# Optimization experiments

Hardware: AMD Instinct MI355X
Metric: run time of the kernel (lower is better)

The kernel has to match this reference:

```python
import jax, jax.numpy as jnp
import numpy as np

N_TOKEN = 267735
D_EMBED = 1024
D_PROJ = 1024
DIV_VAL = 4
CUTOFF_ENDS = [0, 20000, 40000, 200000, N_TOKEN]
EMB_SCALE = D_PROJ ** 0.5
INIT_STD = 0.02


def setup_inputs() -> dict:
    key = jax.random.key(0)
    ks = jax.random.split(key, 9)
    inp = jax.random.randint(ks[0], (4, 4096), 0, N_TOKEN, dtype=jnp.int32)
    out = {"inp": inp}
    for i in range(4):
        l, r = CUTOFF_ENDS[i], CUTOFF_ENDS[i + 1]
        d_i = D_EMBED // DIV_VAL ** i  # 1024, 256, 64, 16
        tbl = jax.random.normal(ks[1 + i], (r - l, d_i), dtype=jnp.float32)
        # padding_idx=1: row 1 is zero-initialized in torch nn.Embedding
        tbl = tbl.at[1].set(0.0)
        out[f"emb{i}"] = tbl
        out[f"proj{i}"] = jax.random.normal(ks[5 + i], (D_PROJ, d_i), dtype=jnp.float32) * INIT_STD
    return out


def reference(inp, emb0, emb1, emb2, emb3, proj0, proj1, proj2, proj3):
    tables = [emb0, emb1, emb2, emb3]
    projs = [proj0, proj1, proj2, proj3]
    flat = inp.reshape(-1)                                  # [N]
    out = jnp.zeros((flat.shape[0], D_PROJ), dtype=emb0.dtype)
    for i in range(4):
        l, r = CUTOFF_ENDS[i], CUTOFF_ENDS[i + 1]
        mask = (flat >= l) & (flat < r)                     # [N] bool
        local = jnp.clip(flat - l, 0, r - l - 1)            # in-range local idx
        e_i = tables[i][local]                              # [N, d_i] gather
        p_i = jnp.einsum('nd,pd->np', e_i, projs[i])        # [N, D_PROJ]
        out = out + jnp.where(mask[:, None], p_i, 0.0)      # scatter-by-mask
    out = out * EMB_SCALE
    return out.reshape(*inp.shape, D_PROJ)
```

## Files before the change

kernel.cpp:

```cpp
#include <hip/hip_runtime.h>
#include <hip/hip_bf16.h>

#define DPROJ 1024

typedef float  f32x4  __attribute__((ext_vector_type(4)));
typedef short  bf16x8 __attribute__((ext_vector_type(8)));

__device__ __forceinline__ unsigned pk2(float a, float b) {
    __hip_bfloat162 h = __float22bfloat162_rn(make_float2(a, b));
    unsigned r; __builtin_memcpy(&r, &h, 4); return r;
}

__global__ __launch_bounds__(1024) void k_classify(
    const int* __restrict__ inp, int n,
    int* __restrict__ cnt, int* __restrict__ lists)
{
    __shared__ uint2 s[1024];
    const int tid = threadIdx.x;
    const int pt  = (n + 1023) >> 10;
    const int t0  = tid * pt;

    int v[16];
    unsigned cp = 0;
    uint2 mine = make_uint2(0u, 0u);
    for (int j = 0; j < pt; ++j) {
        int t = t0 + j, c = 0;
        if (t < n) {
            int x = inp[t]; v[j] = x;
            c = (x >= 20000) + (x >= 40000) + (x >= 200000);
            if      (c == 0) mine.x += 1u;
            else if (c == 1) mine.x += 1u << 16;
            else if (c == 2) mine.y += 1u;
            else             mine.y += 1u << 16;
        } else v[j] = 0;
        cp |= (unsigned)c << (2 * j);
    }
    s[tid] = mine;
    for (int off = 1; off < 1024; off <<= 1) {
        __syncthreads();
        uint2 add = make_uint2(0u, 0u);
        if (tid >= off) add = s[tid - off];
        __syncthreads();
        s[tid].x += add.x; s[tid].y += add.y;
    }
    __syncthreads();
    uint2 tot = s[1023];
    uint2 inc = s[tid];
    unsigned run[4] = { (inc.x & 0xffffu) - (mine.x & 0xffffu),
                        (inc.x >> 16)     - (mine.x >> 16),
                        (inc.y & 0xffffu) - (mine.y & 0xffffu),
                        (inc.y >> 16)     - (mine.y >> 16) };
    if (tid == 0) {
        cnt[0] = (int)(tot.x & 0xffffu); cnt[1] = (int)(tot.x >> 16);
        cnt[2] = (int)(tot.y & 0xffffu); cnt[3] = (int)(tot.y >> 16);
    }
    const int cut[4] = {0, 20000, 40000, 200000};
    for (int j = 0; j < pt; ++j) {
        int t = t0 + j;
        if (t >= n) break;
        int c = (int)((cp >> (2 * j)) & 3u);
        int l = v[j] - cut[c];
        unsigned pos = run[c]++;
        lists[c * n + (int)pos] = (int)(((unsigned)t << 18) | (unsigned)l);
    }
}

__global__ __launch_bounds__(256, 4) void k_gemm(
    const int* __restrict__ cnt, const int* __restrict__ lists, int n,
    const float* __restrict__ e0, const float* __restrict__ p0,
    const float* __restrict__ e1, const float* __restrict__ p1,
    const float* __restrict__ e2, const float* __restrict__ p2,
    const float* __restrict__ e3, const float* __restrict__ p3,
    float* __restrict__ out)
{
    constexpr int TM = 64, TN = 128, KC = 32, STR = 40;

    const int z     = blockIdx.z;
    const int count = cnt[z];
    const int row0  = blockIdx.y * TM;
    if (row0 >= count) return;

    const float* emb  = (z == 0) ? e0 : (z == 1) ? e1 : (z == 2) ? e2 : e3;
    const float* proj = (z == 0) ? p0 : (z == 1) ? p1 : (z == 2) ? p2 : p3;
    const int    K    = (z == 0) ? 1024 : (z == 1) ? 256 : (z == 2) ? 64 : 16;
    const int*   list = lists + (size_t)z * n;
    const int    col0 = blockIdx.x * TN;

    __shared__ int   s_tok[TM];
    __shared__ int   s_loc[TM];
    __shared__ short e_s[TM * STR];
    __shared__ short p_s[TN * STR];

    const int tid = threadIdx.x;
    if (tid < TM) {
        int r = row0 + tid;
        if (r < count) {
            unsigned pk = (unsigned)list[r];
            s_tok[tid] = (int)(pk >> 18);
            s_loc[tid] = (int)(pk & 0x3FFFFu);
        } else { s_tok[tid] = -1; s_loc[tid] = -1; }
    }
    __syncthreads();

    const int  erow = tid >> 2, egrp = tid & 3;
    const int  eloc = s_loc[erow];
    const bool ev   = (eloc >= 0);
    const size_t ebase = ev ? (size_t)eloc * K : 0;

    const int wave = tid >> 6, lane = tid & 63;
    const int lm = lane & 15, quad = lane >> 4;

    f32x4 acc[8];
    #pragma unroll
    for (int i = 0; i < 8; ++i) acc[i] = (f32x4){0.f, 0.f, 0.f, 0.f};

    for (int kb = 0; kb < K; kb += KC) {
        if (kb) __syncthreads();

        {
            float f[8] = {0.f, 0.f, 0.f, 0.f, 0.f, 0.f, 0.f, 0.f};
            int ko = kb + egrp * 8;
            if (ev && ko < K) {
                float4 a = *(const float4*)&emb[ebase + ko];
                float4 b = *(const float4*)&emb[ebase + ko + 4];
                f[0] = a.x; f[1] = a.y; f[2] = a.z; f[3] = a.w;
                f[4] = b.x; f[5] = b.y; f[6] = b.z; f[7] = b.w;
            }
            uint4 q; q.x = pk2(f[0], f[1]); q.y = pk2(f[2], f[3]);
                     q.z = pk2(f[4], f[5]); q.w = pk2(f[6], f[7]);
            *(uint4*)&e_s[erow * STR + egrp * 8] = q;
        }
        #pragma unroll
        for (int it = 0; it < 2; ++it) {
            int u    = tid + it * 256;
            int prow = u >> 2, pgrp = u & 3;
            int ko   = kb + pgrp * 8;
            float f[8] = {0.f, 0.f, 0.f, 0.f, 0.f, 0.f, 0.f, 0.f};
            if (ko < K) {
                const float* src = &proj[(size_t)(col0 + prow) * K + ko];
                float4 a = *(const float4*)src;
                float4 b = *(const float4*)(src + 4);
                f[0] = a.x; f[1] = a.y; f[2] = a.z; f[3] = a.w;
                f[4] = b.x; f[5] = b.y; f[6] = b.z; f[7] = b.w;
            }
            uint4 q; q.x = pk2(f[0], f[1]); q.y = pk2(f[2], f[3]);
                     q.z = pk2(f[4], f[5]); q.w = pk2(f[6], f[7]);
            *(uint4*)&p_s[prow * STR + pgrp * 8] = q;
        }
        __syncthreads();

        bf16x8 af = *(const bf16x8*)&e_s[(wave * 16 + lm) * STR + quad * 8];
        #pragma unroll
        for (int ns = 0; ns < 8; ++ns) {
            bf16x8 bf = *(const bf16x8*)&p_s[(ns * 16 + lm) * STR + quad * 8];
            acc[ns] = __builtin_amdgcn_mfma_f32_16x16x32_bf16(af, bf, acc[ns], 0, 0, 0);
        }
    }

    int toks[4];
    #pragma unroll
    for (int r = 0; r < 4; ++r) toks[r] = s_tok[wave * 16 + quad * 4 + r];
    #pragma unroll
    for (int ns = 0; ns < 8; ++ns) {
        int col = col0 + ns * 16 + lm;
        #pragma unroll
        for (int r = 0; r < 4; ++r) {
            if (toks[r] >= 0)
                out[(size_t)toks[r] * DPROJ + col] = acc[ns][r] * 32.f;
        }
    }
}

extern "C" void kernel_launch(void* const* d_in, const int* in_sizes, int n_in,
                              void* d_out, int out_size, void* d_ws, size_t ws_size,
                              hipStream_t stream) {
    const int*   inp = (const int*)d_in[0];
    const float* e0  = (const float*)d_in[1];
    const float* p0  = (const float*)d_in[2];
    const float* e1  = (const float*)d_in[3];
    const float* p1  = (const float*)d_in[4];
    const float* e2  = (const float*)d_in[5];
    const float* p2  = (const float*)d_in[6];
    const float* e3  = (const float*)d_in[7];
    const float* p3  = (const float*)d_in[8];
    float* out = (float*)d_out;
    const int n = in_sizes[0];

    int* cnt   = (int*)d_ws;
    int* lists = cnt + 4;

    k_classify<<<1, 1024, 0, stream>>>(inp, n, cnt, lists);

    dim3 grid(DPROJ / 128, (n + 63) / 64, 4);
    k_gemm<<<grid, 256, 0, stream>>>(cnt, lists, n, e0, p0, e1, p1, e2, p2, e3, p3, out);
}
```

Before: 262.6 us.

## Parallelize token bucketing, pre-convert projections to bf16, double-buffer GEMM loads

```diff
diff --git a/kernel.cpp b/kernel.cpp
--- a/kernel.cpp
+++ b/kernel.cpp
@@ -11,85 +11,86 @@
     unsigned r; __builtin_memcpy(&r, &h, 4); return r;
 }
 
-__global__ __launch_bounds__(1024) void k_classify(
+__device__ __forceinline__ void gll16(const void* g, void* l) {
+    __builtin_amdgcn_global_load_lds(
+        (const __attribute__((address_space(1))) void*)g,
+        (__attribute__((address_space(3))) void*)l, 16, 0, 0);
+}
+
+__global__ __launch_bounds__(256) void k_prep(
     const int* __restrict__ inp, int n,
-    int* __restrict__ cnt, int* __restrict__ lists)
+    int* __restrict__ cnt, int* __restrict__ lists,
+    const float* __restrict__ p0, const float* __restrict__ p1,
+    const float* __restrict__ p2, const float* __restrict__ p3,
+    short* __restrict__ pb0, short* __restrict__ pb1,
+    short* __restrict__ pb2, short* __restrict__ pb3)
 {
-    __shared__ uint2 s[1024];
     const int tid = threadIdx.x;
-    const int pt  = (n + 1023) >> 10;
-    const int t0  = tid * pt;
-
-    int v[16];
-    unsigned cp = 0;
-    uint2 mine = make_uint2(0u, 0u);
-    for (int j = 0; j < pt; ++j) {
-        int t = t0 + j, c = 0;
+    const int b   = blockIdx.x;
+    const int CB  = (n + 255) >> 8;
+    if (b < CB) {
+        const int t = b * 256 + tid;
+        int c = -1, l = 0;
         if (t < n) {
-            int x = inp[t]; v[j] = x;
+            const int x = inp[t];
             c = (x >= 20000) + (x >= 40000) + (x >= 200000);
-            if      (c == 0) mine.x += 1u;
-            else if (c == 1) mine.x += 1u << 16;
-            else if (c == 2) mine.y += 1u;
-            else             mine.y += 1u << 16;
-        } else v[j] = 0;
-        cp |= (unsigned)c << (2 * j);
-    }
-    s[tid] = mine;
-    for (int off = 1; off < 1024; off <<= 1) {
-        __syncthreads();
-        uint2 add = make_uint2(0u, 0u);
-        if (tid >= off) add = s[tid - off];
-        __syncthreads();
-        s[tid].x += add.x; s[tid].y += add.y;
-    }
-    __syncthreads();
-    uint2 tot = s[1023];
-    uint2 inc = s[tid];
-    unsigned run[4] = { (inc.x & 0xffffu) - (mine.x & 0xffffu),
-                        (inc.x >> 16)     - (mine.x >> 16),
-                        (inc.y & 0xffffu) - (mine.y & 0xffffu),
-                        (inc.y >> 16)     - (mine.y >> 16) };
-    if (tid == 0) {
-        cnt[0] = (int)(tot.x & 0xffffu); cnt[1] = (int)(tot.x >> 16);
-        cnt[2] = (int)(tot.y & 0xffffu); cnt[3] = (int)(tot.y >> 16);
-    }
-    const int cut[4] = {0, 20000, 40000, 200000};
-    for (int j = 0; j < pt; ++j) {
-        int t = t0 + j;
-        if (t >= n) break;
-        int c = (int)((cp >> (2 * j)) & 3u);
-        int l = v[j] - cut[c];
-        unsigned pos = run[c]++;
-        lists[c * n + (int)pos] = (int)(((unsigned)t << 18) | (unsigned)l);
+            l = x - ((c == 0) ? 0 : (c == 1) ? 20000 : (c == 2) ? 40000 : 200000);
+        }
+        const int lane = tid & 63;
+        int pos = 0;
+        #pragma unroll
+        for (int cc = 0; cc < 4; ++cc) {
+            const unsigned long long mk = __ballot(c == cc);
+            if (c == cc) {
+                const int lead = __ffsll(mk) - 1;
+                int base = 0;
+                if (lane == lead) base = atomicAdd(&cnt[cc], (int)__popcll(mk));
+                base = __shfl(base, lead);
+                pos  = base + (int)__popcll(mk & ((1ull << lane) - 1ull));
+            }
+        }
+        if (t < n) lists[c * n + pos] = (int)(((unsigned)t << 18) | (unsigned)l);
+    } else {
+        const long g = (long)(b - CB) * 256 + tid;
+        const float* src; short* dst; long lo;
+        if      (g < 131072) { src = p0; dst = pb0; lo = g; }
+        else if (g < 163840) { src = p1; dst = pb1; lo = g - 131072; }
+        else if (g < 172032) { src = p2; dst = pb2; lo = g - 163840; }
+        else if (g < 174080) { src = p3; dst = pb3; lo = g - 172032; }
+        else return;
+        const float4 a = *(const float4*)(src + lo * 8);
+        const float4 c4 = *(const float4*)(src + lo * 8 + 4);
+        uint4 q; q.x = pk2(a.x, a.y);   q.y = pk2(a.z, a.w);
+                 q.z = pk2(c4.x, c4.y); q.w = pk2(c4.z, c4.w);
+        *(uint4*)(dst + lo * 8) = q;
     }
 }
 
 __global__ __launch_bounds__(256, 4) void k_gemm(
     const int* __restrict__ cnt, const int* __restrict__ lists, int n,
-    const float* __restrict__ e0, const float* __restrict__ p0,
-    const float* __restrict__ e1, const float* __restrict__ p1,
-    const float* __restrict__ e2, const float* __restrict__ p2,
-    const float* __restrict__ e3, const float* __restrict__ p3,
+    const float* __restrict__ e0, const float* __restrict__ e1,
+    const float* __restrict__ e2, const float* __restrict__ e3,
+    const short* __restrict__ pb0, const short* __restrict__ pb1,
+    const short* __restrict__ pb2, const short* __restrict__ pb3,
     float* __restrict__ out)
 {
-    constexpr int TM = 64, TN = 128, KC = 32, STR = 40;
+    constexpr int TM = 64, TN = 128, KC = 32, ESTR = 40;
 
     const int z     = blockIdx.z;
     const int count = cnt[z];
     const int row0  = blockIdx.y * TM;
     if (row0 >= count) return;
 
-    const float* emb  = (z == 0) ? e0 : (z == 1) ? e1 : (z == 2) ? e2 : e3;
-    const float* proj = (z == 0) ? p0 : (z == 1) ? p1 : (z == 2) ? p2 : p3;
-    const int    K    = (z == 0) ? 1024 : (z == 1) ? 256 : (z == 2) ? 64 : 16;
-    const int*   list = lists + (size_t)z * n;
-    const int    col0 = blockIdx.x * TN;
+    const float* emb = (z == 0) ? e0  : (z == 1) ? e1  : (z == 2) ? e2  : e3;
+    const short* pb  = (z == 0) ? pb0 : (z == 1) ? pb1 : (z == 2) ? pb2 : pb3;
+    const int    K   = (z == 0) ? 1024 : (z == 1) ? 256 : (z == 2) ? 64 : 16;
+    const int*  list = lists + (size_t)z * n;
+    const int   col0 = blockIdx.x * TN;
 
     __shared__ int   s_tok[TM];
     __shared__ int   s_loc[TM];
-    __shared__ short e_s[TM * STR];
-    __shared__ short p_s[TN * STR];
+    __shared__ short e_s[2][TM * ESTR];
+    __shared__ short p_s[2][4 * TN * 8];
 
     const int tid = threadIdx.x;
     if (tid < TM) {
@@ -102,71 +103,93 @@
     }
     __syncthreads();
 
-    const int  erow = tid >> 2, egrp = tid & 3;
-    const int  eloc = s_loc[erow];
-    const bool ev   = (eloc >= 0);
-    const size_t ebase = ev ? (size_t)eloc * K : 0;
-
     const int wave = tid >> 6, lane = tid & 63;
     const int lm = lane & 15, quad = lane >> 4;
+
+    const int erow = tid >> 2, egrp = tid & 3;
+    const int eloc = s_loc[erow];
+    const bool ev  = (eloc >= 0);
+    const float* ebase = emb + (ev ? (size_t)eloc * K : 0) + egrp * 8;
+    const int eoff = erow * ESTR + egrp * 8;
+    short* ebuf = (short*)e_s;
+    short* pbuf = (short*)p_s;
+
+    const short* pg0 = pb + (size_t)(col0 +      lane) * K + wave * 8;
+    const short* pg1 = pb + (size_t)(col0 + 64 + lane) * K + wave * 8;
+    const int pdoff0 = wave * 128 * 8;
+    const int pdoff1 = wave * 128 * 8 + 64 * 8;
 
     f32x4 acc[8];
     #pragma unroll
     for (int i = 0; i < 8; ++i) acc[i] = (f32x4){0.f, 0.f, 0.f, 0.f};
 
-    for (int kb = 0; kb < K; kb += KC) {
-        if (kb) __syncthreads();
-
-        {
-            float f[8] = {0.f, 0.f, 0.f, 0.f, 0.f, 0.f, 0.f, 0.f};
-            int ko = kb + egrp * 8;
-            if (ev && ko < K) {
-                float4 a = *(const float4*)&emb[ebase + ko];
-                float4 b = *(const float4*)&emb[ebase + ko + 4];
-                f[0] = a.x; f[1] = a.y; f[2] = a.z; f[3] = a.w;
-                f[4] = b.x; f[5] = b.y; f[6] = b.z; f[7] = b.w;
+    const int nt = (K + KC - 1) / KC;
+    float ef[8];
+
+    {
+        const bool v = ev && (egrp * 8 < K);
+        if (v) {
+            float4 a = *(const float4*)(ebase);
+            float4 b = *(const float4*)(ebase + 4);
+            ef[0] = a.x; ef[1] = a.y; ef[2] = a.z; ef[3] = a.w;
+            ef[4] = b.x; ef[5] = b.y; ef[6] = b.z; ef[7] = b.w;
+        } else {
+            #pragma unroll
+            for (int j = 0; j < 8; ++j) ef[j] = 0.f;
+        }
+        gll16(pg0, pbuf + pdoff0);
+        gll16(pg1, pbuf + pdoff1);
+        uint4 q; q.x = pk2(ef[0], ef[1]); q.y = pk2(ef[2], ef[3]);
+                 q.z = pk2(ef[4], ef[5]); q.w = pk2(ef[6], ef[7]);
+        *(uint4*)(ebuf + eoff) = q;
+    }
+    __syncthreads();
+
+    for (int t = 0; t < nt; ++t) {
+        const int  cur = t & 1;
+        const int  kn  = (t + 1) * KC;
+        const bool pf  = (kn < K);
+        if (pf) {
+            const bool v = ev && (kn + egrp * 8 < K);
+            if (v) {
+                const float* s = ebase + kn;
+                float4 a = *(const float4*)(s);
+                float4 b = *(const float4*)(s + 4);
+                ef[0] = a.x; ef[1] = a.y; ef[2] = a.z; ef[3] = a.w;
+                ef[4] = b.x; ef[5] = b.y; ef[6] = b.z; ef[7] = b.w;
+            } else {
+                #pragma unroll
+                for (int j = 0; j < 8; ++j) ef[j] = 0.f;
             }
-            uint4 q; q.x = pk2(f[0], f[1]); q.y = pk2(f[2], f[3]);
-                     q.z = pk2(f[4], f[5]); q.w = pk2(f[6], f[7]);
-            *(uint4*)&e_s[erow * STR + egrp * 8] = q;
-        }
-        #pragma unroll
-        for (int it = 0; it < 2; ++it) {
-            int u    = tid + it * 256;
-            int prow = u >> 2, pgrp = u & 3;
-            int ko   = kb + pgrp * 8;
-            float f[8] = {0.f, 0.f, 0.f, 0.f, 0.f, 0.f, 0.f, 0.f};
-            if (ko < K) {
-                const float* src = &proj[(size_t)(col0 + prow) * K + ko];
-                float4 a = *(const float4*)src;
-                float4 b = *(const float4*)(src + 4);
-                f[0] = a.x; f[1] = a.y; f[2] = a.z; f[3] = a.w;
-                f[4] = b.x; f[5] = b.y; f[6] = b.z; f[7] = b.w;
-            }
-            uint4 q; q.x = pk2(f[0], f[1]); q.y = pk2(f[2], f[3]);
-                     q.z = pk2(f[4], f[5]); q.w = pk2(f[6], f[7]);
-            *(uint4*)&p_s[prow * STR + pgrp * 8] = q;
-        }
-        __syncthreads();
-
-        bf16x8 af = *(const bf16x8*)&e_s[(wave * 16 + lm) * STR + quad * 8];
+            const int nb = (cur ^ 1) * 4096;
+            gll16(pg0 + kn, pbuf + nb + pdoff0);
+            gll16(pg1 + kn, pbuf + nb + pdoff1);
+        }
+
+        bf16x8 ebf = *(const bf16x8*)(ebuf + cur * (TM * ESTR)
+                                      + (wave * 16 + lm) * ESTR + quad * 8);
+        const short* pk_ = pbuf + cur * 4096 + quad * (TN * 8) + lm * 8;
         #pragma unroll
         for (int ns = 0; ns < 8; ++ns) {
-            bf16x8 bf = *(const bf16x8*)&p_s[(ns * 16 + lm) * STR + quad * 8];
-            acc[ns] = __builtin_amdgcn_mfma_f32_16x16x32_bf16(af, bf, acc[ns], 0, 0, 0);
-        }
-    }
-
-    int toks[4];
-    #pragma unroll
-    for (int r = 0; r < 4; ++r) toks[r] = s_tok[wave * 16 + quad * 4 + r];
-    #pragma unroll
-    for (int ns = 0; ns < 8; ++ns) {
-        int col = col0 + ns * 16 + lm;
+            bf16x8 pfr = *(const bf16x8*)(pk_ + ns * 128);
+            acc[ns] = __builtin_amdgcn_mfma_f32_16x16x32_bf16(pfr, ebf, acc[ns], 0, 0, 0);
+        }
+
+        if (pf) {
+            uint4 q; q.x = pk2(ef[0], ef[1]); q.y = pk2(ef[2], ef[3]);
+                     q.z = pk2(ef[4], ef[5]); q.w = pk2(ef[6], ef[7]);
+            *(uint4*)(ebuf + (cur ^ 1) * (TM * ESTR) + eoff) = q;
+        }
+        __syncthreads();
+    }
+
+    const int tok = s_tok[wave * 16 + lm];
+    if (tok >= 0) {
+        float* orow = out + (size_t)tok * DPROJ + col0 + quad * 4;
         #pragma unroll
-        for (int r = 0; r < 4; ++r) {
-            if (toks[r] >= 0)
-                out[(size_t)toks[r] * DPROJ + col] = acc[ns][r] * 32.f;
+        for (int ns = 0; ns < 8; ++ns) {
+            f32x4 v = acc[ns] * 32.f;
+            __builtin_nontemporal_store(v, (f32x4*)(orow + ns * 16));
         }
     }
 }
@@ -186,11 +209,23 @@
     float* out = (float*)d_out;
     const int n = in_sizes[0];
 
-    int* cnt   = (int*)d_ws;
-    int* lists = cnt + 4;
-
-    k_classify<<<1, 1024, 0, stream>>>(inp, n, cnt, lists);
+    char* wsb  = (char*)d_ws;
+    int* cnt   = (int*)wsb;
+    int* lists = (int*)(wsb + 16);
+    size_t off = 16 + (size_t)4 * n * sizeof(int);
+    off = (off + 255) & ~(size_t)255;
+    short* pb0 = (short*)(wsb + off); off += (size_t)1024 * 1024 * 2;
+    short* pb1 = (short*)(wsb + off); off += (size_t)1024 * 256 * 2;
+    short* pb3 = (short*)(wsb + off); off += (size_t)1024 * 16 * 2;
+    short* pb2 = (short*)(wsb + off); off += (size_t)1024 * 64 * 2;
+
+    hipMemsetAsync(cnt, 0, 4 * sizeof(int), stream);
+
+    const int CB = (n + 255) >> 8;
+    k_prep<<<CB + 680, 256, 0, stream>>>(inp, n, cnt, lists,
+                                         p0, p1, p2, p3, pb0, pb1, pb2, pb3);
 
     dim3 grid(DPROJ / 128, (n + 63) / 64, 4);
-    k_gemm<<<grid, 256, 0, stream>>>(cnt, lists, n, e0, p0, e1, p1, e2, p2, e3, p3, out);
-}
+    k_gemm<<<grid, 256, 0, stream>>>(cnt, lists, n, e0, e1, e2, e3,
+                                     pb0, pb1, pb2, pb3, out);
+}
```

After: 234.5 us. -10.7%, faster.
